# Performance work log

Measured on AMD Instinct MI355X. Metric: run time of the kernel, lower is better.

Reference implementation:

```python
import jax, jax.numpy as jnp
import numpy as np

THRESHOLD = 2.0 / 3.0


def _quantize_1_58_bit(weight):
    """BitNet b1.58: ternary {-1,0,+1} * scale, scale = mean(|w|) clamped."""
    scale = jnp.clip(jnp.mean(jnp.abs(weight)), 1e-5, 1000.0)
    weight_norm = jnp.clip(weight / scale, -10.0, 10.0)
    q = jnp.where(weight_norm > THRESHOLD, 1.0,
                  jnp.where(weight_norm < -THRESHOLD, -1.0, 0.0)).astype(weight.dtype)
    return q, scale


def setup_inputs() -> dict:
    key = jax.random.key(0)
    k1, k2 = jax.random.split(key)
    B, S, D_IN, D_OUT = 4, 2048, 4096, 4096
    x = jax.random.normal(k1, (B, S, D_IN), dtype=jnp.float32)
    weight = jax.random.normal(k2, (D_OUT, D_IN), dtype=jnp.float32)
    bias = jnp.zeros((D_OUT,), dtype=jnp.float32)
    return {"x": x, "weight": weight, "bias": bias}


def reference(x, weight, bias):
    # Training-path forward value == eval-path forward value:
    # dequantized ternary weight, F.linear semantics (x @ W.T + b).
    q, scale = _quantize_1_58_bit(weight)
    weight_q = q * scale  # [out, in]
    out = jnp.einsum('bsi,oi->bso', x, weight_q) + bias
    return out
```

## Files before the change

kernel.cpp:

```cpp
#include <hip/hip_runtime.h>
#include <hip/hip_bf16.h>
#include <stdint.h>


#define BM 128
#define BN 128
#define BK 64

typedef __bf16 bf16x8 __attribute__((ext_vector_type(8)));
typedef float f32x4 __attribute__((ext_vector_type(4)));

__device__ __forceinline__ unsigned short f2bf_rne(float f) {
  union { float f; unsigned int u; } v; v.f = f;
  unsigned int u = v.u;
  u += 0x7FFFu + ((u >> 16) & 1u);
  return (unsigned short)(u >> 16);
}

__global__ void absum_kernel(const float4* __restrict__ w, int n4,
                             double* __restrict__ out) {
  float s = 0.f;
  for (int i = blockIdx.x * blockDim.x + threadIdx.x; i < n4;
       i += gridDim.x * blockDim.x) {
    float4 v = w[i];
    s += fabsf(v.x) + fabsf(v.y) + fabsf(v.z) + fabsf(v.w);
  }
#pragma unroll
  for (int off = 32; off > 0; off >>= 1) s += __shfl_down(s, off);
  __shared__ float partial[4];
  if ((threadIdx.x & 63) == 0) partial[threadIdx.x >> 6] = s;
  __syncthreads();
  if (threadIdx.x == 0)
    atomicAdd(out, (double)(partial[0] + partial[1] + partial[2] + partial[3]));
}

__global__ void quant_kernel(const float4* __restrict__ w, int n4,
                             const double* __restrict__ sum, double inv_cnt,
                             ushort4* __restrict__ q) {
  float scale = (float)fmin(fmax(sum[0] * inv_cnt, 1e-5), 1000.0);
  const float T = 2.0f / 3.0f;
  for (int i = blockIdx.x * blockDim.x + threadIdx.x; i < n4;
       i += gridDim.x * blockDim.x) {
    float4 v = w[i];
    ushort4 o;
    float nx = v.x / scale, ny = v.y / scale, nz = v.z / scale, nw = v.w / scale;
    o.x = (nx > T) ? 0x3F80u : ((nx < -T) ? 0xBF80u : 0u);
    o.y = (ny > T) ? 0x3F80u : ((ny < -T) ? 0xBF80u : 0u);
    o.z = (nz > T) ? 0x3F80u : ((nz < -T) ? 0xBF80u : 0u);
    o.w = (nw > T) ? 0x3F80u : ((nw < -T) ? 0xBF80u : 0u);
    q[i] = o;
  }
}

__global__ void xcvt_kernel(const float4* __restrict__ x, int n4,
                            ushort4* __restrict__ xb) {
  for (int i = blockIdx.x * blockDim.x + threadIdx.x; i < n4;
       i += gridDim.x * blockDim.x) {
    float4 v = x[i];
    ushort4 o;
    o.x = f2bf_rne(v.x);
    o.y = f2bf_rne(v.y);
    o.z = f2bf_rne(v.z);
    o.w = f2bf_rne(v.w);
    xb[i] = o;
  }
}

__global__ void gemm_kernel(const ushort* __restrict__ xb,
                            const ushort* __restrict__ qb,
                            const float* __restrict__ bias,
                            const double* __restrict__ sum,
                            float* __restrict__ out,
                            int M, int N, int K, double inv_cnt) {
  __shared__ __align__(16) ushort As[BM * BK];
  __shared__ __align__(16) ushort Bs[BN * BK];

  const int t = threadIdx.x;
  const int wave = t >> 6;
  const int lane = t & 63;
  const int m0 = blockIdx.y * BM;
  const int n0 = blockIdx.x * BN;

  const int wr = (wave >> 1) * 64;
  const int wc = (wave & 1) * 64;
  const int lm = lane & 15;
  const int lk = lane >> 4;

  const int srow = lane >> 3;
  const int scol = (lane & 7) * 8;
  const ushort* ag = xb + (size_t)(m0 + wave * 32 + srow) * K + scol;
  const ushort* bg = qb + (size_t)(n0 + wave * 32 + srow) * K + scol;
  ushort* al = &As[(wave * 32) * BK];
  ushort* bl = &Bs[(wave * 32) * BK];

  f32x4 acc[4][4] = {};

  for (int k0 = 0; k0 < K; k0 += BK) {
#pragma unroll
    for (int s = 0; s < 4; ++s) {
      __builtin_amdgcn_global_load_lds(
          (const __attribute__((address_space(1))) void*)(ag + (size_t)s * 8 * K),
          (__attribute__((address_space(3))) void*)(al + s * 8 * BK), 16, 0, 0);
      __builtin_amdgcn_global_load_lds(
          (const __attribute__((address_space(1))) void*)(bg + (size_t)s * 8 * K),
          (__attribute__((address_space(3))) void*)(bl + s * 8 * BK), 16, 0, 0);
    }
    __syncthreads();

#pragma unroll
    for (int ks = 0; ks < 2; ++ks) {
      bf16x8 af[4], bf[4];
#pragma unroll
      for (int i = 0; i < 4; ++i)
        af[i] = *(const bf16x8*)&As[(wr + i * 16 + lm) * BK + ks * 32 + lk * 8];
#pragma unroll
      for (int j = 0; j < 4; ++j)
        bf[j] = *(const bf16x8*)&Bs[(wc + j * 16 + lm) * BK + ks * 32 + lk * 8];
#pragma unroll
      for (int i = 0; i < 4; ++i)
#pragma unroll
        for (int j = 0; j < 4; ++j)
          acc[i][j] = __builtin_amdgcn_mfma_f32_16x16x32_bf16(af[i], bf[j],
                                                             acc[i][j], 0, 0, 0);
    }
    __syncthreads();
    ag += BK;
    bg += BK;
  }

  float scale = (float)fmin(fmax(sum[0] * inv_cnt, 1e-5), 1000.0);

#pragma unroll
  for (int j = 0; j < 4; ++j) {
    const int col = n0 + wc + j * 16 + lm;
    const float bv = bias[col];
#pragma unroll
    for (int i = 0; i < 4; ++i) {
      const int row = m0 + wr + i * 16 + lk * 4;
      float* op = out + (size_t)row * N + col;
#pragma unroll
      for (int r = 0; r < 4; ++r)
        op[(size_t)r * N] = acc[i][j][r] * scale + bv;
    }
  }
}

extern "C" void kernel_launch(void* const* d_in, const int* in_sizes, int n_in,
                              void* d_out, int out_size, void* d_ws,
                              size_t ws_size, hipStream_t stream) {
  const float* x = (const float*)d_in[0];
  const float* w = (const float*)d_in[1];
  const float* bias = (const float*)d_in[2];
  float* out = (float*)d_out;

  const int DOUT = in_sizes[2];
  const int DIN = in_sizes[1] / DOUT;
  const int M = in_sizes[0] / DIN;
  const int N = DOUT, K = DIN;

  char* ws = (char*)d_ws;
  double* sum = (double*)ws;
  ushort* xb = (ushort*)(ws + 256);
  ushort* qb = (ushort*)(ws + 256 + (size_t)M * K * 2);

  const double inv_cnt = 1.0 / ((double)N * (double)K);

  hipMemsetAsync(d_ws, 0, 8, stream);

  const int wn4 = (N * K) / 4;
  absum_kernel<<<1024, 256, 0, stream>>>((const float4*)w, wn4, sum);
  quant_kernel<<<2048, 256, 0, stream>>>((const float4*)w, wn4, sum, inv_cnt,
                                         (ushort4*)qb);
  const int xn4 = (M * K) / 4;
  xcvt_kernel<<<4096, 256, 0, stream>>>((const float4*)x, xn4, (ushort4*)xb);

  dim3 grid(N / BN, M / BM);
  gemm_kernel<<<grid, 256, 0, stream>>>(xb, qb, bias, sum, out, M, N, K,
                                        inv_cnt);
}
```

Measured before the change: 566.2 us.

## Swizzle GEMM LDS tiles with XOR and widen conversion kernels to 8 elements

The GEMM's LDS tile layout gets an XOR swizzle: each lane's 16-byte global chunk lands in a permuted slot, and fragment reads use the matching XOR. The aim is to remove LDS bank conflicts on the bf16x8 fragment loads, where the row stride is 128 bytes. The quantize and convert kernels now handle 8 elements per thread with 16-byte stores, and prep-kernel grid sizes are doubled. The swizzle must stay consistent between the global-load source address and the read index, otherwise results are wrong.

```diff
diff --git a/kernel.cpp b/kernel.cpp
--- a/kernel.cpp
+++ b/kernel.cpp
@@ -9,6 +9,7 @@
 
 typedef __bf16 bf16x8 __attribute__((ext_vector_type(8)));
 typedef float f32x4 __attribute__((ext_vector_type(4)));
+typedef unsigned short u16x8 __attribute__((ext_vector_type(8)));
 
 __device__ __forceinline__ unsigned short f2bf_rne(float f) {
   union { float f; unsigned int u; } v; v.f = f;
@@ -34,34 +35,34 @@
     atomicAdd(out, (double)(partial[0] + partial[1] + partial[2] + partial[3]));
 }
 
-__global__ void quant_kernel(const float4* __restrict__ w, int n4,
+__global__ void quant_kernel(const float4* __restrict__ w, int n8,
                              const double* __restrict__ sum, double inv_cnt,
-                             ushort4* __restrict__ q) {
+                             u16x8* __restrict__ q) {
   float scale = (float)fmin(fmax(sum[0] * inv_cnt, 1e-5), 1000.0);
   const float T = 2.0f / 3.0f;
-  for (int i = blockIdx.x * blockDim.x + threadIdx.x; i < n4;
+  for (int i = blockIdx.x * blockDim.x + threadIdx.x; i < n8;
        i += gridDim.x * blockDim.x) {
-    float4 v = w[i];
-    ushort4 o;
-    float nx = v.x / scale, ny = v.y / scale, nz = v.z / scale, nw = v.w / scale;
-    o.x = (nx > T) ? 0x3F80u : ((nx < -T) ? 0xBF80u : 0u);
-    o.y = (ny > T) ? 0x3F80u : ((ny < -T) ? 0xBF80u : 0u);
-    o.z = (nz > T) ? 0x3F80u : ((nz < -T) ? 0xBF80u : 0u);
-    o.w = (nw > T) ? 0x3F80u : ((nw < -T) ? 0xBF80u : 0u);
+    float4 a = w[2 * i], b = w[2 * i + 1];
+    float f[8] = {a.x, a.y, a.z, a.w, b.x, b.y, b.z, b.w};
+    u16x8 o;
+#pragma unroll
+    for (int j = 0; j < 8; ++j) {
+      float n = f[j] / scale;
+      o[j] = (n > T) ? 0x3F80u : ((n < -T) ? 0xBF80u : 0u);
+    }
     q[i] = o;
   }
 }
 
-__global__ void xcvt_kernel(const float4* __restrict__ x, int n4,
-                            ushort4* __restrict__ xb) {
-  for (int i = blockIdx.x * blockDim.x + threadIdx.x; i < n4;
+__global__ void xcvt_kernel(const float4* __restrict__ x, int n8,
+                            u16x8* __restrict__ xb) {
+  for (int i = blockIdx.x * blockDim.x + threadIdx.x; i < n8;
        i += gridDim.x * blockDim.x) {
-    float4 v = x[i];
-    ushort4 o;
-    o.x = f2bf_rne(v.x);
-    o.y = f2bf_rne(v.y);
-    o.z = f2bf_rne(v.z);
-    o.w = f2bf_rne(v.w);
+    float4 a = x[2 * i], b = x[2 * i + 1];
+    float f[8] = {a.x, a.y, a.z, a.w, b.x, b.y, b.z, b.w};
+    u16x8 o;
+#pragma unroll
+    for (int j = 0; j < 8; ++j) o[j] = f2bf_rne(f[j]);
     xb[i] = o;
   }
 }
@@ -87,9 +88,9 @@
   const int lk = lane >> 4;
 
   const int srow = lane >> 3;
-  const int scol = (lane & 7) * 8;
-  const ushort* ag = xb + (size_t)(m0 + wave * 32 + srow) * K + scol;
-  const ushort* bg = qb + (size_t)(n0 + wave * 32 + srow) * K + scol;
+  const int schunk = (lane & 7) ^ srow;
+  const ushort* ag = xb + (size_t)(m0 + wave * 32 + srow) * K + schunk * 8;
+  const ushort* bg = qb + (size_t)(n0 + wave * 32 + srow) * K + schunk * 8;
   ushort* al = &As[(wave * 32) * BK];
   ushort* bl = &Bs[(wave * 32) * BK];
 
@@ -111,11 +112,17 @@
     for (int ks = 0; ks < 2; ++ks) {
       bf16x8 af[4], bf[4];
 #pragma unroll
-      for (int i = 0; i < 4; ++i)
-        af[i] = *(const bf16x8*)&As[(wr + i * 16 + lm) * BK + ks * 32 + lk * 8];
+      for (int i = 0; i < 4; ++i) {
+        const int row = wr + i * 16 + lm;
+        const int slot = (ks * 4 + lk) ^ (lm & 7);
+        af[i] = *(const bf16x8*)&As[row * BK + slot * 8];
+      }
 #pragma unroll
-      for (int j = 0; j < 4; ++j)
-        bf[j] = *(const bf16x8*)&Bs[(wc + j * 16 + lm) * BK + ks * 32 + lk * 8];
+      for (int j = 0; j < 4; ++j) {
+        const int row = wc + j * 16 + lm;
+        const int slot = (ks * 4 + lk) ^ (lm & 7);
+        bf[j] = *(const bf16x8*)&Bs[row * BK + slot * 8];
+      }
 #pragma unroll
       for (int i = 0; i < 4; ++i)
 #pragma unroll
@@ -168,11 +175,12 @@
   hipMemsetAsync(d_ws, 0, 8, stream);
 
   const int wn4 = (N * K) / 4;
-  absum_kernel<<<1024, 256, 0, stream>>>((const float4*)w, wn4, sum);
-  quant_kernel<<<2048, 256, 0, stream>>>((const float4*)w, wn4, sum, inv_cnt,
-                                         (ushort4*)qb);
-  const int xn4 = (M * K) / 4;
-  xcvt_kernel<<<4096, 256, 0, stream>>>((const float4*)x, xn4, (ushort4*)xb);
+  const int wn8 = (N * K) / 8;
+  absum_kernel<<<2048, 256, 0, stream>>>((const float4*)w, wn4, sum);
+  quant_kernel<<<4096, 256, 0, stream>>>((const float4*)w, wn8, sum, inv_cnt,
+                                         (u16x8*)qb);
+  const int xn8 = (M * K) / 8;
+  xcvt_kernel<<<8192, 256, 0, stream>>>((const float4*)x, xn8, (u16x8*)xb);
 
   dim3 grid(N / BN, M / BM);
   gemm_kernel<<<grid, 256, 0, stream>>>(xb, qb, bias, sum, out, M, N, K,
```

Measured after the change: 541.1 us. 4.4% less time.
